# Optimization experiments

Hardware: AMD Instinct MI355X
Metric: run time of the kernel (lower is better)

## Reference

```python
import jax, jax.numpy as jnp
import numpy as np

EMBED_DIM = 1024
NUM_HEADS = 16
HEAD_DIM = EMBED_DIM // NUM_HEADS
EPS = 1e-6


def setup_inputs() -> dict:
    key = jax.random.key(0)
    ks = jax.random.split(key, 11)
    Lq, Lk, N = 4096, 4096, 4
    s = 1.0 / np.sqrt(EMBED_DIM)
    inp = {
        'q': jax.random.normal(ks[0], (Lq, N, EMBED_DIM), dtype=jnp.float32),
        'k': jax.random.normal(ks[1], (Lk, N, EMBED_DIM), dtype=jnp.float32),
        'v': jax.random.normal(ks[2], (Lk, N, EMBED_DIM), dtype=jnp.float32),
        'Wq': jax.random.normal(ks[3], (EMBED_DIM, EMBED_DIM), dtype=jnp.float32) * s,
        'bq': jax.random.normal(ks[4], (EMBED_DIM,), dtype=jnp.float32) * s,
        'Wk': jax.random.normal(ks[5], (EMBED_DIM, EMBED_DIM), dtype=jnp.float32) * s,
        'bk': jax.random.normal(ks[6], (EMBED_DIM,), dtype=jnp.float32) * s,
        'Wv': jax.random.normal(ks[7], (EMBED_DIM, EMBED_DIM), dtype=jnp.float32) * s,
        'bv': jax.random.normal(ks[8], (EMBED_DIM,), dtype=jnp.float32) * s,
        'Wo': jax.random.normal(ks[9], (EMBED_DIM, EMBED_DIM), dtype=jnp.float32) * s,
        'bo': jax.random.normal(ks[10], (EMBED_DIM,), dtype=jnp.float32) * s,
    }
    return inp


def _feature_map(x):
    # F.elu(x) + 1
    return jax.nn.elu(x) + 1.0


def reference(q, k, v, Wq, bq, Wk, bk, Wv, bv, Wo, bo):
    Lq, N, E = q.shape
    Lk = k.shape[0]
    # torch Linear: y = x @ W.T + b
    qp = q @ Wq.T + bq
    kp = k @ Wk.T + bk
    vp = v @ Wv.T + bv
    # (L, N, E) -> (N, H, L, D)
    qh = qp.reshape(Lq, N, NUM_HEADS, HEAD_DIM).transpose(1, 2, 0, 3)
    kh = kp.reshape(Lk, N, NUM_HEADS, HEAD_DIM).transpose(1, 2, 0, 3)
    vh = vp.reshape(Lk, N, NUM_HEADS, HEAD_DIM).transpose(1, 2, 0, 3)
    qf = _feature_map(qh)
    kf = _feature_map(kh)
    k_sum = kf.sum(axis=2)                               # (N, H, D)
    kv = jnp.einsum('nhld,nhle->nhde', kf, vh)            # (N, H, D, D)
    z = 1.0 / (jnp.einsum('nhld,nhd->nhl', qf, k_sum) + EPS)
    out = jnp.einsum('nhld,nhde->nhle', qf, kv) * z[..., None]
    out = out.transpose(2, 0, 1, 3).reshape(Lq, N, E)
    out = out @ Wo.T + bo
    return out
```

## Files before the change

### kernel.cpp

```cpp
#include <hip/hip_runtime.h>
#include <hip/hip_bf16.h>
#include <cstdint>


typedef __attribute__((ext_vector_type(8))) short bf16x8;
typedef __attribute__((ext_vector_type(4))) float f32x4;

#define L_SEQ 4096
#define NBATCH 4
#define EMB 1024
#define NHEADS 16
#define HDIM 64
#define MROWS (L_SEQ * NBATCH)
#define NHG (NBATCH * NHEADS)
#define LCHUNK 512
#define NCHUNK (L_SEQ / LCHUNK)

__device__ __forceinline__ unsigned short f2bf(float f) {
  union { float f; uint32_t u; } v; v.f = f;
  uint32_t u = v.u;
  u += 0x7fffu + ((u >> 16) & 1u);
  return (unsigned short)(u >> 16);
}
__device__ __forceinline__ float bf2f(unsigned short s) {
  union { uint32_t u; float f; } v; v.u = ((uint32_t)s) << 16;
  return v.f;
}
__device__ __forceinline__ uint32_t pkbf(float a, float b) {
  union { float f; uint32_t u; } ua, ub; ua.f = a; ub.f = b;
  return ((ua.u + 0x8000u) >> 16) | ((ub.u + 0x8000u) & 0xffff0000u);
}

__global__ __launch_bounds__(256) void convert_kernel(const float* __restrict__ src,
                                                      unsigned short* __restrict__ dst,
                                                      int n) {
  int i = (blockIdx.x * 256 + threadIdx.x) * 4;
  if (i + 4 <= n) {
    float4 f = *(const float4*)(src + i);
    uint2 p;
    p.x = pkbf(f.x, f.y);
    p.y = pkbf(f.z, f.w);
    *(uint2*)(dst + i) = p;
  }
}

__global__ __launch_bounds__(256) void convert_w4(const float* __restrict__ s0,
                                                  const float* __restrict__ s1,
                                                  const float* __restrict__ s2,
                                                  const float* __restrict__ s3,
                                                  unsigned short* __restrict__ d0,
                                                  unsigned short* __restrict__ d1,
                                                  unsigned short* __restrict__ d2,
                                                  unsigned short* __restrict__ d3,
                                                  int n) {
  const int w = blockIdx.y;
  const float* src = (w == 0) ? s0 : (w == 1) ? s1 : (w == 2) ? s2 : s3;
  unsigned short* dst = (w == 0) ? d0 : (w == 1) ? d1 : (w == 2) ? d2 : d3;
  int i = (blockIdx.x * 256 + threadIdx.x) * 4;
  if (i + 4 <= n) {
    float4 f = *(const float4*)(src + i);
    uint2 p;
    p.x = pkbf(f.x, f.y);
    p.y = pkbf(f.z, f.w);
    *(uint2*)(dst + i) = p;
  }
}


#define STAGE_HALF(SB, H, KTN)                                                  \
  do {                                                                          \
    _Pragma("unroll")                                                           \
    for (int r_ = 0; r_ < 2; r_++) {                                            \
      const long grow_ = ((H) < 2 ? arow0 + (H) * 128 : bcol0 + ((H)-2) * 128)  \
                         + r_ * 64 + srowt;                                     \
      const unsigned short* gp_ =                                               \
          ((H) < 2 ? A : B) + grow_ * (long)K + (KTN) + skoff;                  \
      __builtin_amdgcn_global_load_lds(                                         \
          (const __attribute__((address_space(1))) void*)gp_,                   \
          (__attribute__((address_space(3))) void*)(smem + (SB) + (H) * 16384 + \
                                                    r_ * 8192 + wid * 1024),    \
          16, 0, 0);                                                            \
    }                                                                           \
  } while (0)

#define MFMA_Q(AF, BF, MFB, NFB)                                                \
  do {                                                                          \
    __builtin_amdgcn_s_setprio(1);                                              \
    _Pragma("unroll")                                                           \
    for (int mi_ = 0; mi_ < 4; mi_++)                                           \
      _Pragma("unroll")                                                         \
      for (int ni_ = 0; ni_ < 2; ni_++)                                         \
        _Pragma("unroll")                                                       \
        for (int ks_ = 0; ks_ < 2; ks_++)                                       \
          acc[(MFB) + mi_][(NFB) + ni_] =                                       \
              __builtin_amdgcn_mfma_f32_16x16x32_bf16(                          \
                  AF[mi_ * 2 + ks_], BF[ni_ * 2 + ks_],                         \
                  acc[(MFB) + mi_][(NFB) + ni_], 0, 0, 0);                      \
    __builtin_amdgcn_s_setprio(0);                                              \
  } while (0)

#define PH_SYNC                                                                 \
  __builtin_amdgcn_s_barrier();                                                 \
  asm volatile("s_waitcnt lgkmcnt(0)" ::: "memory");                            \
  __builtin_amdgcn_sched_barrier(0);

#define TILE(RB, SB, KTN, DOSTG)                                                \
  do {                                                                          \
    bf16x8 af0[8], af1[8], bf0[4], bf1[4];                                      \
                              \
    _Pragma("unroll")                                                           \
    for (int mi_ = 0; mi_ < 4; mi_++)                                           \
      _Pragma("unroll")                                                         \
      for (int ks_ = 0; ks_ < 2; ks_++)                                         \
        af0[mi_ * 2 + ks_] = *(const bf16x8*)(smem + (RB) + aRowBase +          \
                                              mi_ * 2048 + akt[ks_]);           \
    _Pragma("unroll")                                                           \
    for (int ni_ = 0; ni_ < 2; ni_++)                                           \
      _Pragma("unroll")                                                         \
      for (int ks_ = 0; ks_ < 2; ks_++)                                         \
        bf0[ni_ * 2 + ks_] = *(const bf16x8*)(smem + (RB) + bRowBase +          \
                                              ni_ * 2048 + akt[ks_]);           \
    if (DOSTG) STAGE_HALF(SB, 0, KTN);                                          \
    PH_SYNC                                                                     \
    MFMA_Q(af0, bf0, 0, 0);                                                     \
    __builtin_amdgcn_s_barrier();                                               \
                                     \
    _Pragma("unroll")                                                           \
    for (int ni_ = 0; ni_ < 2; ni_++)                                           \
      _Pragma("unroll")                                                         \
      for (int ks_ = 0; ks_ < 2; ks_++)                                         \
        bf1[ni_ * 2 + ks_] = *(const bf16x8*)(smem + (RB) + bRowBase +          \
                                              (ni_ + 2) * 2048 + akt[ks_]);     \
    if (DOSTG) STAGE_HALF(SB, 1, KTN);                                          \
    PH_SYNC                                                                     \
    MFMA_Q(af0, bf1, 0, 2);                                                     \
    __builtin_amdgcn_s_barrier();                                               \
                                     \
    _Pragma("unroll")                                                           \
    for (int mi_ = 0; mi_ < 4; mi_++)                                           \
      _Pragma("unroll")                                                         \
      for (int ks_ = 0; ks_ < 2; ks_++)                                         \
        af1[mi_ * 2 + ks_] = *(const bf16x8*)(smem + (RB) + aRowBase +          \
                                              (mi_ + 4) * 2048 + akt[ks_]);     \
    if (DOSTG) STAGE_HALF(SB, 2, KTN);                                          \
    PH_SYNC                                                                     \
    MFMA_Q(af1, bf1, 4, 2);                                                     \
    __builtin_amdgcn_s_barrier();                                               \
                        \
    if (DOSTG) STAGE_HALF(SB, 3, KTN);                                          \
    PH_SYNC                                                                     \
    MFMA_Q(af1, bf0, 4, 0);                                                     \
    if (DOSTG) asm volatile("s_waitcnt vmcnt(0)" ::: "memory");                 \
    __builtin_amdgcn_s_barrier();                                               \
  } while (0)

template <int MODE>
__global__ __launch_bounds__(512, 2) void gemm_bt(const unsigned short* __restrict__ A,
                                                  const unsigned short* __restrict__ B,
                                                  const float* __restrict__ bias,
                                                  void* __restrict__ Cout,
                                                  int M, int Nn, int K) {
  __shared__ __align__(16) char smem[131072];

  const int tid   = threadIdx.x;
  const int wid   = tid >> 6;
  const int lane  = tid & 63;
  const int col16 = lane & 15;
  const int quad  = lane >> 4;
  const int wr = wid >> 2;
  const int wc = wid & 3;
  const long arow0 = (long)blockIdx.x * 256;
  const long bcol0 = (long)blockIdx.y * 256;

  const int axor = (col16 & 7) << 4;
  int akt[2];
  akt[0] = (quad * 16) ^ axor;
  akt[1] = (64 + quad * 16) ^ axor;
  const int aRowBase = wr * 16384 + col16 * 128;
  const int bRowBase = 32768 + (wc >> 1) * 16384 + ((wc & 1) * 64 + col16) * 128;

  const int srowt = tid >> 3;
  const int skoff = (((tid & 7) * 16) ^ ((srowt & 7) << 4)) >> 1;

  const int NT = K >> 6;

  STAGE_HALF(0, 0, 0);
  STAGE_HALF(0, 1, 0);
  STAGE_HALF(0, 2, 0);
  STAGE_HALF(0, 3, 0);

  const f32x4 fzero = {0.f, 0.f, 0.f, 0.f};
  f32x4 acc[8][4];
#pragma unroll
  for (int i = 0; i < 8; i++)
#pragma unroll
    for (int j = 0; j < 4; j++) acc[i][j] = fzero;

  asm volatile("s_waitcnt vmcnt(0)" ::: "memory");
  __builtin_amdgcn_s_barrier();

#pragma unroll 1
  for (int u = 0; u + 4 <= NT; u += 2) {
    TILE(0, 65536, (u + 1) * 64, 1);
    TILE(65536, 0, (u + 2) * 64, 1);
  }
  TILE(0, 65536, (NT - 1) * 64, 1);
  TILE(65536, 0, 0, 0);

  float bcol[4];
#pragma unroll
  for (int nf = 0; nf < 4; nf++) bcol[nf] = bias[bcol0 + wc * 64 + nf * 16 + col16];

  const int erow = tid >> 4;
  const int ecc  = tid & 15;

  if (MODE != 2) {
    unsigned short* epi = (unsigned short*)smem;
    const int EST = 264;
#pragma unroll
    for (int s = 0; s < 8; s++) {
      if ((s >> 2) == wr) {
        const int mfb = (s & 3) * 2;
#pragma unroll
        for (int ml = 0; ml < 2; ml++)
#pragma unroll
          for (int nf = 0; nf < 4; nf++)
#pragma unroll
            for (int rr = 0; rr < 4; rr++) {
              float vv = acc[mfb + ml][nf][rr] + bcol[nf];
              if (MODE == 0) vv = (vv > 0.f) ? (vv + 1.f) : __expf(vv);
              epi[(ml * 16 + quad * 4 + rr) * EST + wc * 64 + nf * 16 + col16] =
                  f2bf(vv);
            }
      }
      __syncthreads();
      {
        const long gr = arow0 + s * 32 + erow;
        const unsigned short* srcp = &epi[erow * EST + ecc * 16];
        uint4 a  = *(const uint4*)srcp;
        uint4 b2 = *(const uint4*)(srcp + 8);
        unsigned short* Cp = (unsigned short*)Cout + gr * Nn + bcol0 + ecc * 16;
        *(uint4*)Cp       = a;
        *(uint4*)(Cp + 8) = b2;
      }
      __syncthreads();
    }
  } else {
    float* epi = (float*)smem;
    const int ESF = 260;
#pragma unroll
    for (int s = 0; s < 8; s++) {
      if ((s >> 2) == wr) {
        const int mfb = (s & 3) * 2;
#pragma unroll
        for (int ml = 0; ml < 2; ml++)
#pragma unroll
          for (int nf = 0; nf < 4; nf++)
#pragma unroll
            for (int rr = 0; rr < 4; rr++)
              epi[(ml * 16 + quad * 4 + rr) * ESF + wc * 64 + nf * 16 + col16] =
                  acc[mfb + ml][nf][rr] + bcol[nf];
      }
      __syncthreads();
      {
        const long gr = arow0 + s * 32 + erow;
        const float* srcp = &epi[erow * ESF + ecc * 16];
        float* Cp = (float*)Cout + gr * Nn + bcol0 + ecc * 16;
#pragma unroll
        for (int s4 = 0; s4 < 4; s4++)
          *(float4*)(Cp + s4 * 4) = *(const float4*)(srcp + s4 * 4);
      }
      __syncthreads();
    }
  }
}

__global__ __launch_bounds__(256) void kv_partial_kernel(const unsigned short* __restrict__ kf,
                                                         const unsigned short* __restrict__ vp,
                                                         float* __restrict__ kvp,
                                                         float* __restrict__ ksp) {
  __shared__ float ks[32 * 64];
  __shared__ float vs[32 * 64];
  const int hg = blockIdx.x;
  const int chunk = blockIdx.y;
  const int n = hg >> 4, h = hg & 15;
  const int tid = threadIdx.x;
  const int td = tid >> 4, te = tid & 15;
  const long hoff = (long)n * EMB + h * HDIM;
  const int l0 = chunk * LCHUNK;

  float acc[4][4];
#pragma unroll
  for (int i = 0; i < 4; i++)
#pragma unroll
    for (int j = 0; j < 4; j++) acc[i][j] = 0.f;
  float ksacc[4] = {0.f, 0.f, 0.f, 0.f};

  const int lrow = tid >> 3;
  const int dcol = (tid & 7) * 8;

  for (int ls = 0; ls < LCHUNK; ls += 32) {
    const long g = (long)(l0 + ls + lrow) * (NBATCH * EMB) + hoff + dcol;
    uint4 kr = *(const uint4*)(kf + g);
    uint4 vr = *(const uint4*)(vp + g);
    float* kd = &ks[lrow * 64 + dcol];
    float* vd = &vs[lrow * 64 + dcol];
    uint32_t ku[4] = {kr.x, kr.y, kr.z, kr.w};
    uint32_t vu[4] = {vr.x, vr.y, vr.z, vr.w};
#pragma unroll
    for (int t2 = 0; t2 < 4; t2++) {
      kd[2 * t2]     = bf2f((unsigned short)(ku[t2] & 0xffffu));
      kd[2 * t2 + 1] = bf2f((unsigned short)(ku[t2] >> 16));
      vd[2 * t2]     = bf2f((unsigned short)(vu[t2] & 0xffffu));
      vd[2 * t2 + 1] = bf2f((unsigned short)(vu[t2] >> 16));
    }
    __syncthreads();
#pragma unroll
    for (int l = 0; l < 32; l++) {
      float kq[4], vq[4];
      *(float4*)kq = *(const float4*)(&ks[l * 64 + td * 4]);
      *(float4*)vq = *(const float4*)(&vs[l * 64 + te * 4]);
#pragma unroll
      for (int i = 0; i < 4; i++) {
        ksacc[i] += kq[i];
#pragma unroll
        for (int j = 0; j < 4; j++) acc[i][j] += kq[i] * vq[j];
      }
    }
    __syncthreads();
  }
  float* outp = kvp + ((long)chunk * NHG + hg) * 4096;
#pragma unroll
  for (int i = 0; i < 4; i++)
#pragma unroll
    for (int j = 0; j < 4; j++)
      outp[(td * 4 + i) * 64 + te * 4 + j] = acc[i][j];
  if (te == 0) {
    float* o2 = ksp + ((long)chunk * NHG + hg) * 64;
#pragma unroll
    for (int i = 0; i < 4; i++) o2[td * 4 + i] = ksacc[i];
  }
}

__global__ __launch_bounds__(256) void attn_out_kernel(const unsigned short* __restrict__ qf,
                                                       const float* __restrict__ kvp,
                                                       const float* __restrict__ ksp,
                                                       unsigned short* __restrict__ out1) {
  __shared__ __align__(16) char smem[53248];
  const int hg = blockIdx.x;
  const int lc = blockIdx.y;
  const int n = hg >> 4, h = hg & 15;
  const int tid = threadIdx.x;
  const int wid = tid >> 6;
  const int lane = tid & 63;
  const int col16 = lane & 15;
  const int quad  = lane >> 4;
  const long lbase = (long)lc * 256;

#pragma unroll
  for (int r = 0; r < 8; r++) {
    const int row = r * 32 + (tid >> 3);
    const long l = lbase + row;
    const int sk = (((tid & 7) * 16) ^ ((row & 7) << 4)) >> 1;
    const unsigned short* gp = qf + (l * NBATCH + n) * (long)EMB + h * HDIM + sk;
    __builtin_amdgcn_global_load_lds(
        (const __attribute__((address_space(1))) void*)gp,
        (__attribute__((address_space(3))) void*)(smem + r * 4096 + tid * 16),
        16, 0, 0);
  }

  char* Bl = smem + 32768;
  for (int w = tid; w < 4096; w += 256) {
    const int d = w >> 6, e = w & 63;
    float s = 0.f;
#pragma unroll
    for (int c = 0; c < NCHUNK; c++) s += kvp[((long)c * NHG + hg) * 4096 + w];
    const unsigned short hi = f2bf(s);
    const unsigned short lo = f2bf(s - bf2f(hi));
    const int key = (e & 7) << 4;
    *(unsigned short*)(Bl + e * 256 + ((2 * d) ^ key))       = hi;
    *(unsigned short*)(Bl + e * 256 + ((128 + 2 * d) ^ key)) = lo;
  }
  if (tid < 64) {
    float s = 0.f;
#pragma unroll
    for (int c = 0; c < NCHUNK; c++) s += ksp[((long)c * NHG + hg) * 64 + tid];
    const unsigned short hi = f2bf(s);
    const unsigned short lo = f2bf(s - bf2f(hi));
    *(unsigned short*)(Bl + 64 * 256 + 2 * tid)       = hi;
    *(unsigned short*)(Bl + 64 * 256 + 128 + 2 * tid) = lo;
  }
  {
    uint32_t* zb = (uint32_t*)(Bl + 65 * 256);
    for (int i = tid; i < 15 * 64; i += 256) zb[i] = 0u;
  }
  __syncthreads();

  const int wl0 = wid * 64;
  const int akey = (col16 & 7) << 4;

  bf16x8 af[4][2];
#pragma unroll
  for (int mi = 0; mi < 4; mi++)
#pragma unroll
    for (int ks = 0; ks < 2; ks++)
      af[mi][ks] = *(const bf16x8*)(smem + (wl0 + mi * 16 + col16) * 128 +
                                    ((ks * 64 + quad * 16) ^ akey));

  const f32x4 fzero = {0.f, 0.f, 0.f, 0.f};
  f32x4 acc[4][5];
#pragma unroll
  for (int mi = 0; mi < 4; mi++)
#pragma unroll
    for (int nf = 0; nf < 5; nf++) acc[mi][nf] = fzero;

#pragma unroll
  for (int nf = 0; nf < 5; nf++) {
    bf16x8 bfr[4];
#pragma unroll
    for (int pass = 0; pass < 2; pass++)
#pragma unroll
      for (int ks = 0; ks < 2; ks++)
        bfr[pass * 2 + ks] = *(const bf16x8*)(Bl + (nf * 16 + col16) * 256 +
                                              ((pass * 128 + ks * 64 + quad * 16) ^ akey));
#pragma unroll
    for (int mi = 0; mi < 4; mi++)
#pragma unroll
      for (int pass = 0; pass < 2; pass++)
#pragma unroll
        for (int ks = 0; ks < 2; ks++)
          acc[mi][nf] = __builtin_amdgcn_mfma_f32_16x16x32_bf16(
              af[mi][ks], bfr[pass * 2 + ks], acc[mi][nf], 0, 0, 0);
  }

  __syncthreads();

  unsigned short* epi = (unsigned short*)smem;
#pragma unroll
  for (int mi = 0; mi < 4; mi++) {
#pragma unroll
    for (int rr = 0; rr < 4; rr++) {
      const float dv = __shfl(acc[mi][4][rr], lane & 48);
      const float z = 1.f / (dv + 1e-6f);
      const int row = wl0 + mi * 16 + quad * 4 + rr;
      const int key = (row & 7) << 4;
#pragma unroll
      for (int nf = 0; nf < 4; nf++)
        *(unsigned short*)((char*)epi + row * 128 +
                           (((nf * 16 + col16) * 2) ^ key)) =
            f2bf(acc[mi][nf][rr] * z);
    }
  }
  __syncthreads();

#pragma unroll
  for (int r = 0; r < 8; r++) {
    const int row = r * 32 + (tid >> 3);
    const long l = lbase + row;
    const uint4 vv = *(const uint4*)((char*)epi + row * 128 +
                                     (((tid & 7) * 16) ^ ((row & 7) << 4)));
    *(uint4*)(out1 + (l * NBATCH + n) * (long)EMB + h * HDIM + (tid & 7) * 8) = vv;
  }
}

extern "C" void kernel_launch(void* const* d_in, const int* in_sizes, int n_in,
                              void* d_out, int out_size, void* d_ws, size_t ws_size,
                              hipStream_t stream) {
  const float* q  = (const float*)d_in[0];
  const float* k  = (const float*)d_in[1];
  const float* v  = (const float*)d_in[2];
  const float* Wq = (const float*)d_in[3];
  const float* bq = (const float*)d_in[4];
  const float* Wk = (const float*)d_in[5];
  const float* bk = (const float*)d_in[6];
  const float* Wv = (const float*)d_in[7];
  const float* bv = (const float*)d_in[8];
  const float* Wo = (const float*)d_in[9];
  const float* bo = (const float*)d_in[10];

  char* ws = (char*)d_ws;
  const size_t BUF = (size_t)MROWS * EMB * 2;
  unsigned short* T0  = (unsigned short*)(ws);
  unsigned short* qf  = (unsigned short*)(ws + BUF);
  unsigned short* kf  = (unsigned short*)(ws + 2 * BUF);
  unsigned short* vp  = (unsigned short*)(ws + 3 * BUF);
  unsigned short* Wqb = (unsigned short*)(ws + 4 * BUF);
  unsigned short* Wkb = Wqb + (size_t)EMB * EMB;
  unsigned short* Wvb = Wkb + (size_t)EMB * EMB;
  unsigned short* Wob = Wvb + (size_t)EMB * EMB;
  float* kvp = (float*)(ws + 4 * BUF + 4 * (size_t)EMB * EMB * 2);
  float* ksp = kvp + (size_t)NCHUNK * NHG * HDIM * HDIM;

  const int nQKV = MROWS * EMB;
  const int nW   = EMB * EMB;

  convert_w4<<<dim3(nW / 1024, 4), 256, 0, stream>>>(Wq, Wk, Wv, Wo,
                                                     Wqb, Wkb, Wvb, Wob, nW);

  dim3 gg(MROWS / 256, EMB / 256), bb(512);

  convert_kernel<<<nQKV / 1024, 256, 0, stream>>>(q, T0, nQKV);
  gemm_bt<0><<<gg, bb, 0, stream>>>(T0, Wqb, bq, qf, MROWS, EMB, EMB);
  convert_kernel<<<nQKV / 1024, 256, 0, stream>>>(k, T0, nQKV);
  gemm_bt<0><<<gg, bb, 0, stream>>>(T0, Wkb, bk, kf, MROWS, EMB, EMB);
  convert_kernel<<<nQKV / 1024, 256, 0, stream>>>(v, T0, nQKV);
  gemm_bt<1><<<gg, bb, 0, stream>>>(T0, Wvb, bv, vp, MROWS, EMB, EMB);

  kv_partial_kernel<<<dim3(NHG, NCHUNK), 256, 0, stream>>>(kf, vp, kvp, ksp);
  attn_out_kernel<<<dim3(NHG, L_SEQ / 256), 256, 0, stream>>>(qf, kvp, ksp, T0);

  gemm_bt<2><<<gg, bb, 0, stream>>>(T0, Wob, bo, d_out, MROWS, EMB, EMB);
}
```

Before: 481.5 us.

## Split GEMM LDS staging into row-half slots for deeper prefetch

Reorganizes the shared-memory layout of the bf16 GEMM into four 16KB row-half slots per matrix and stages halves of the next two K-tiles in a rotating pattern. Each half is loaded as soon as it is free rather than a whole tile ahead, and the end-of-tile wait becomes vmcnt(4) instead of a full drain. The aim is to keep global loads in flight across tile boundaries and hide memory latency behind MFMA work. The slot rotation and partial waits are easy to get wrong and could cause reads of stale LDS data.

```diff
diff --git a/kernel.cpp b/kernel.cpp
--- a/kernel.cpp
+++ b/kernel.cpp
@@ -67,18 +67,17 @@
 }
 
 
-#define STAGE_HALF(SB, H, KTN)                                                  \
+#define STAGE_H(MATB, RH, SLOT, KTN)                                            \
   do {                                                                          \
     _Pragma("unroll")                                                           \
     for (int r_ = 0; r_ < 2; r_++) {                                            \
-      const long grow_ = ((H) < 2 ? arow0 + (H) * 128 : bcol0 + ((H)-2) * 128)  \
-                         + r_ * 64 + srowt;                                     \
+      const long grow_ = ((MATB) ? bcol0 : arow0) + (RH) * 128 + r_ * 64 + srowt;\
       const unsigned short* gp_ =                                               \
-          ((H) < 2 ? A : B) + grow_ * (long)K + (KTN) + skoff;                  \
+          ((MATB) ? B : A) + grow_ * (long)K + (KTN) + skoff;                   \
       __builtin_amdgcn_global_load_lds(                                         \
           (const __attribute__((address_space(1))) void*)gp_,                   \
-          (__attribute__((address_space(3))) void*)(smem + (SB) + (H) * 16384 + \
-                                                    r_ * 8192 + wid * 1024),    \
+          (__attribute__((address_space(3))) void*)(smem + (MATB) * 65536 +     \
+              (SLOT) * 16384 + r_ * 8192 + wid * 1024),                         \
           16, 0, 0);                                                            \
     }                                                                           \
   } while (0)
@@ -104,53 +103,56 @@
   asm volatile("s_waitcnt lgkmcnt(0)" ::: "memory");                            \
   __builtin_amdgcn_sched_barrier(0);
 
-#define TILE(RB, SB, KTN, DOSTG)                                                \
+#define TILE_T(SA, K1, K2, S01, S23, VMODE)                                     \
   do {                                                                          \
     bf16x8 af0[8], af1[8], bf0[4], bf1[4];                                      \
-                              \
+             \
     _Pragma("unroll")                                                           \
     for (int mi_ = 0; mi_ < 4; mi_++)                                           \
       _Pragma("unroll")                                                         \
       for (int ks_ = 0; ks_ < 2; ks_++)                                         \
-        af0[mi_ * 2 + ks_] = *(const bf16x8*)(smem + (RB) + aRowBase +          \
+        af0[mi_ * 2 + ks_] = *(const bf16x8*)(smem + ((SA) + wr) * 16384 + aRB +\
                                               mi_ * 2048 + akt[ks_]);           \
     _Pragma("unroll")                                                           \
     for (int ni_ = 0; ni_ < 2; ni_++)                                           \
       _Pragma("unroll")                                                         \
       for (int ks_ = 0; ks_ < 2; ks_++)                                         \
-        bf0[ni_ * 2 + ks_] = *(const bf16x8*)(smem + (RB) + bRowBase +          \
+        bf0[ni_ * 2 + ks_] = *(const bf16x8*)(smem + 65536 +                    \
+                                              ((SA) + (wc >> 1)) * 16384 + bRB +\
                                               ni_ * 2048 + akt[ks_]);           \
-    if (DOSTG) STAGE_HALF(SB, 0, KTN);                                          \
+    if (S01) STAGE_H(0, 1, (SA) ^ 3, K1);                                       \
     PH_SYNC                                                                     \
     MFMA_Q(af0, bf0, 0, 0);                                                     \
     __builtin_amdgcn_s_barrier();                                               \
-                                     \
+                                      \
     _Pragma("unroll")                                                           \
     for (int ni_ = 0; ni_ < 2; ni_++)                                           \
       _Pragma("unroll")                                                         \
       for (int ks_ = 0; ks_ < 2; ks_++)                                         \
-        bf1[ni_ * 2 + ks_] = *(const bf16x8*)(smem + (RB) + bRowBase +          \
+        bf1[ni_ * 2 + ks_] = *(const bf16x8*)(smem + 65536 +                    \
+                                              ((SA) + (wc >> 1)) * 16384 + bRB +\
                                               (ni_ + 2) * 2048 + akt[ks_]);     \
-    if (DOSTG) STAGE_HALF(SB, 1, KTN);                                          \
+    if (S01) STAGE_H(1, 1, (SA) ^ 3, K1);                                       \
     PH_SYNC                                                                     \
     MFMA_Q(af0, bf1, 0, 2);                                                     \
     __builtin_amdgcn_s_barrier();                                               \
-                                     \
+                                  \
     _Pragma("unroll")                                                           \
     for (int mi_ = 0; mi_ < 4; mi_++)                                           \
       _Pragma("unroll")                                                         \
       for (int ks_ = 0; ks_ < 2; ks_++)                                         \
-        af1[mi_ * 2 + ks_] = *(const bf16x8*)(smem + (RB) + aRowBase +          \
+        af1[mi_ * 2 + ks_] = *(const bf16x8*)(smem + ((SA) + wr) * 16384 + aRB +\
                                               (mi_ + 4) * 2048 + akt[ks_]);     \
-    if (DOSTG) STAGE_HALF(SB, 2, KTN);                                          \
+    if (S23) STAGE_H(1, 0, (SA), K2);                                           \
     PH_SYNC                                                                     \
     MFMA_Q(af1, bf1, 4, 2);                                                     \
     __builtin_amdgcn_s_barrier();                                               \
-                        \
-    if (DOSTG) STAGE_HALF(SB, 3, KTN);                                          \
+                     \
+    if (S23) STAGE_H(0, 0, (SA), K2);                                           \
     PH_SYNC                                                                     \
     MFMA_Q(af1, bf0, 4, 0);                                                     \
-    if (DOSTG) asm volatile("s_waitcnt vmcnt(0)" ::: "memory");                 \
+    if ((VMODE) == 1) asm volatile("s_waitcnt vmcnt(4)" ::: "memory");          \
+    if ((VMODE) == 2) asm volatile("s_waitcnt vmcnt(0)" ::: "memory");          \
     __builtin_amdgcn_s_barrier();                                               \
   } while (0)
 
@@ -176,18 +178,20 @@
   int akt[2];
   akt[0] = (quad * 16) ^ axor;
   akt[1] = (64 + quad * 16) ^ axor;
-  const int aRowBase = wr * 16384 + col16 * 128;
-  const int bRowBase = 32768 + (wc >> 1) * 16384 + ((wc & 1) * 64 + col16) * 128;
+  const int aRB = col16 * 128;
+  const int bRB = ((wc & 1) * 64 + col16) * 128;
 
   const int srowt = tid >> 3;
   const int skoff = (((tid & 7) * 16) ^ ((srowt & 7) << 4)) >> 1;
 
   const int NT = K >> 6;
 
-  STAGE_HALF(0, 0, 0);
-  STAGE_HALF(0, 1, 0);
-  STAGE_HALF(0, 2, 0);
-  STAGE_HALF(0, 3, 0);
+  STAGE_H(0, 0, 0, 0);
+  STAGE_H(0, 1, 1, 0);
+  STAGE_H(1, 0, 0, 0);
+  STAGE_H(1, 1, 1, 0);
+  STAGE_H(1, 0, 2, 64);
+  STAGE_H(0, 0, 2, 64);
 
   const f32x4 fzero = {0.f, 0.f, 0.f, 0.f};
   f32x4 acc[8][4];
@@ -196,16 +200,16 @@
 #pragma unroll
     for (int j = 0; j < 4; j++) acc[i][j] = fzero;
 
-  asm volatile("s_waitcnt vmcnt(0)" ::: "memory");
+  asm volatile("s_waitcnt vmcnt(4)" ::: "memory");
   __builtin_amdgcn_s_barrier();
 
 #pragma unroll 1
   for (int u = 0; u + 4 <= NT; u += 2) {
-    TILE(0, 65536, (u + 1) * 64, 1);
-    TILE(65536, 0, (u + 2) * 64, 1);
-  }
-  TILE(0, 65536, (NT - 1) * 64, 1);
-  TILE(65536, 0, 0, 0);
+    TILE_T(0, (u + 1) * 64, (u + 2) * 64, 1, 1, 1);
+    TILE_T(2, (u + 2) * 64, (u + 3) * 64, 1, 1, 1);
+  }
+  TILE_T(0, (NT - 1) * 64, 0, 1, 0, 2);
+  TILE_T(2, 0, 0, 0, 0, 0);
 
   float bcol[4];
 #pragma unroll
```

New measurement: 461.9 us. 4.1% less time.
